# Kernel tuning notes

Measured on AMD Instinct MI355X. Metric: run time of the kernel, lower is better.

Reference implementation:

```python
import jax, jax.numpy as jnp
import numpy as np

B, S, D, H, MULT = 4, 2048, 768, 12, 4
HD = D // H
EPS = 1e-6


def _ln(x, g, b):
    mu = jnp.mean(x, axis=-1, keepdims=True)
    var = jnp.var(x, axis=-1, keepdims=True)
    return (x - mu) * jax.lax.rsqrt(var + EPS) * g + b


def setup_inputs() -> dict:
    key = jax.random.key(0)
    ks = jax.random.split(key, 12)
    sd = 0.02
    inp = {
        "x": jax.random.normal(ks[0], (B, S, D), dtype=jnp.float32),
        "mask": jnp.ones((B, 1, 1, S), dtype=jnp.int32),
        "Wq": jax.random.normal(ks[1], (D, D), dtype=jnp.float32) * sd,
        "bq": jnp.zeros((D,), dtype=jnp.float32),
        "Wk": jax.random.normal(ks[2], (D, D), dtype=jnp.float32) * sd,
        "bk": jnp.zeros((D,), dtype=jnp.float32),
        "Wv": jax.random.normal(ks[3], (D, D), dtype=jnp.float32) * sd,
        "bv": jnp.zeros((D,), dtype=jnp.float32),
        "Wo": jax.random.normal(ks[4], (D, D), dtype=jnp.float32) * sd,
        "bo": jnp.zeros((D,), dtype=jnp.float32),
        "W1": jax.random.normal(ks[5], (D, MULT * D), dtype=jnp.float32) * sd,
        "b1": jnp.zeros((MULT * D,), dtype=jnp.float32),
        "W2": jax.random.normal(ks[6], (MULT * D, D), dtype=jnp.float32) * sd,
        "b2": jnp.zeros((D,), dtype=jnp.float32),
        "g1": jnp.ones((D,), dtype=jnp.float32),
        "be1": jnp.zeros((D,), dtype=jnp.float32),
        "g2": jnp.ones((D,), dtype=jnp.float32),
        "be2": jnp.zeros((D,), dtype=jnp.float32),
    }
    return inp


def reference(x, mask, Wq, bq, Wk, bk, Wv, bv, Wo, bo, W1, b1, W2, b2, g1, be1, g2, be2):
    scale = HD ** -0.5
    # projections -> [B,H,S,HD]
    q = (x @ Wq + bq).reshape(B, S, H, HD).transpose(0, 2, 1, 3)
    k = (x @ Wk + bk).reshape(B, S, H, HD).transpose(0, 2, 1, 3)
    v = (x @ Wv + bv).reshape(B, S, H, HD).transpose(0, 2, 1, 3)
    scores = jnp.einsum("bhqd,bhkd->bhqk", q, k) * scale
    scores = jnp.where(mask == 0, -jnp.inf, scores)
    attn = jax.nn.softmax(scores, axis=-1)
    out = jnp.einsum("bhqk,bhkd->bhqd", attn, v)
    out = out.transpose(0, 2, 1, 3).reshape(B, S, D)
    mha = out @ Wo + bo
    # residual + LN
    h = _ln(mha + x, g1, be1)
    # FFN (dropout inactive in eval; GELU exact as torch nn.GELU default)
    ff = jax.nn.gelu(h @ W1 + b1, approximate=False) @ W2 + b2
    return _ln(ff + h, g2, be2)
```

## Files before the change

### kernel.cpp

```cpp
#include <hip/hip_runtime.h>
#include <hip/hip_bf16.h>
#include <math.h>

#define B_  4
#define S_  2048
#define D_  768
#define H_  12
#define HD_ 64
#define DF_ 3072
#define BS_ (B_*S_)

#define QSCALE 0.18033688011112042f

typedef __attribute__((ext_vector_type(8))) short short8;
typedef __attribute__((ext_vector_type(4))) float f32x4;

__device__ __forceinline__ unsigned short f2b(float f){
    unsigned int x = __float_as_uint(f);
    return (unsigned short)((x + 0x7fffu + ((x >> 16) & 1u)) >> 16);
}
__device__ __forceinline__ float b2f(unsigned short u){
    return __uint_as_float(((unsigned int)u) << 16);
}

typedef __attribute__((address_space(1))) void gvoid_t;
typedef __attribute__((address_space(3))) void lvoid_t;
__device__ __forceinline__ void gload_lds16(const unsigned short* g, unsigned short* l){
    __builtin_amdgcn_global_load_lds((gvoid_t*)g, (lvoid_t*)l, 16, 0, 0);
}

__global__ __launch_bounds__(256) void prep_kernel(
    const float* __restrict__ x,
    const float* __restrict__ Wq, const float* __restrict__ Wk,
    const float* __restrict__ Wv, const float* __restrict__ Wo,
    const float* __restrict__ W1, const float* __restrict__ W2,
    const float* __restrict__ bq, const float* __restrict__ bk, const float* __restrict__ bv,
    unsigned short* __restrict__ xb, unsigned short* __restrict__ wqkvT,
    unsigned short* __restrict__ woT, unsigned short* __restrict__ w1T,
    unsigned short* __restrict__ w2T, float* __restrict__ bqkv)
{
    const int NCVT = (BS_*D_)/256;
    int bid = blockIdx.x;
    if (bid < NCVT){
        int i = bid*256 + threadIdx.x;
        xb[i] = f2b(x[i]);
        return;
    }
    bid -= NCVT;
    __shared__ float t[32][33];
    const float* src; unsigned short* dst; int K, N, bx, by;
    if (bid < 4*576){
        int wsel = bid / 576, tt = bid % 576;
        bx = tt % 24; by = tt / 24; K = D_; N = D_;
        src = (wsel==0)?Wq:(wsel==1)?Wk:(wsel==2)?Wv:Wo;
        dst = (wsel<3) ? (wqkvT + (size_t)wsel*D_*D_) : woT;
    } else if (bid < 4*576 + 2304){
        int tt = bid - 4*576; bx = tt % 96; by = tt / 96; K = D_; N = DF_; src = W1; dst = w1T;
    } else if (bid < 4*576 + 2*2304){
        int tt = bid - 4*576 - 2304; bx = tt % 24; by = tt / 24; K = DF_; N = D_; src = W2; dst = w2T;
    } else {
        int i = (bid - (4*576 + 2*2304))*256 + threadIdx.x;
        if (i < 3*D_) bqkv[i] = (i < D_) ? bq[i] : (i < 2*D_) ? bk[i-D_] : bv[i-2*D_];
        return;
    }
    int tx = threadIdx.x & 31, ty = threadIdx.x >> 5;
    #pragma unroll
    for (int i = 0; i < 4; ++i)
        t[ty + i*8][tx] = src[(size_t)(by*32 + ty + i*8) * N + bx*32 + tx];
    __syncthreads();
    #pragma unroll
    for (int i = 0; i < 4; ++i)
        dst[(size_t)(bx*32 + ty + i*8) * K + by*32 + tx] = f2b(t[tx][ty + i*8]);
}

__global__ __launch_bounds__(256, 4) void gemm_tn(
    const unsigned short* __restrict__ A,
    const unsigned short* __restrict__ Bt,
    const float* __restrict__ bias,
    float* __restrict__ Cf,
    unsigned short* __restrict__ Cb,
    unsigned short* __restrict__ vtg,
    int M, int N, int K, int klen, int act)
{
    __shared__ __align__(16) unsigned short As[128*64];
    __shared__ __align__(16) unsigned short Bs[128*64];

    const int tid  = threadIdx.x;
    const int bz   = blockIdx.z;
    const int w    = tid >> 6, lane = tid & 63;
    const int l16  = lane & 15, quad = lane >> 4;
    const int wm   = (w >> 1) * 64, wn = (w & 1) * 64;
    const int kbeg = bz * klen;

    const int nwg = gridDim.x * gridDim.y;
    int wg = blockIdx.y * gridDim.x + blockIdx.x;
    wg = (wg & 7) * (nwg >> 3) + (wg >> 3);
    const int bn = wg % gridDim.x, bm = wg / gridDim.x;

    const unsigned short* Abase = A  + (size_t)bm * 128 * K;
    const unsigned short* Bbase = Bt + (size_t)bn * 128 * K;

    f32x4 acc[4][4] = {};

    for (int kt = kbeg; kt < kbeg + klen; kt += 64){
        #pragma unroll
        for (int c0 = 0; c0 < 4; ++c0){
            int c = tid + c0 * 256;
            int row = c >> 3, q = c & 7;
            int sw = (q ^ row) & 7;
            gload_lds16(Abase + (size_t)row * K + kt + sw*8, As + c*8);
            gload_lds16(Bbase + (size_t)row * K + kt + sw*8, Bs + c*8);
        }
        __syncthreads();

        #pragma unroll
        for (int kc = 0; kc < 2; ++kc){
            short8 af[4], bf[4];
            #pragma unroll
            for (int mi = 0; mi < 4; ++mi)
                af[mi] = *(const short8*)&As[(wm + mi*16 + l16)*64 + (((kc*4 + quad) ^ l16) & 7)*8];
            #pragma unroll
            for (int ni = 0; ni < 4; ++ni)
                bf[ni] = *(const short8*)&Bs[(wn + ni*16 + l16)*64 + (((kc*4 + quad) ^ l16) & 7)*8];
            #pragma unroll
            for (int mi = 0; mi < 4; ++mi)
                #pragma unroll
                for (int ni = 0; ni < 4; ++ni)
                    acc[mi][ni] = __builtin_amdgcn_mfma_f32_16x16x32_bf16(af[mi], bf[ni], acc[mi][ni], 0, 0, 0);
        }
        __syncthreads();
    }

    if (act == 2 && bn >= 12){
        #pragma unroll
        for (int mi = 0; mi < 4; ++mi){
            int rowbase = bm*128 + wm + mi*16 + quad*4;
            int bidx = rowbase >> 11, s0 = rowbase & 2047;
            int sp = (s0 & ~31) | (((s0 >> 2) & 3) << 3) | (((s0 >> 4) & 1) << 2);
            #pragma unroll
            for (int ni = 0; ni < 4; ++ni){
                int col  = bn*128 + wn + ni*16 + l16;
                int hcol = col - 2*D_;
                int hh   = hcol >> 6, dd = hcol & 63;
                float bia = bias ? bias[col] : 0.f;
                unsigned long long pk = 0;
                #pragma unroll
                for (int r = 0; r < 4; ++r)
                    pk |= (unsigned long long)f2b(acc[mi][ni][r] + bia) << (16*r);
                *(unsigned long long*)(vtg + (((size_t)bidx*H_ + hh)*64 + dd)*2048 + sp) = pk;
            }
        }
        return;
    }

    float* Cfz = Cf ? (Cf + (size_t)bz * M * N) : nullptr;
    const bool addb = (bias != nullptr) && (bz == 0);
    #pragma unroll
    for (int mi = 0; mi < 4; ++mi){
        #pragma unroll
        for (int ni = 0; ni < 4; ++ni){
            int col = bn*128 + wn + ni*16 + l16;
            float bia = addb ? bias[col] : 0.f;
            #pragma unroll
            for (int r = 0; r < 4; ++r){
                int row = bm*128 + wm + mi*16 + quad*4 + r;
                float v = acc[mi][ni][r] + bia;
                if (act == 1){
                    float u = v * (0.7978845608028654f + 0.0356774081f * v * v);
                    float e = __builtin_amdgcn_exp2f(u * 2.885390081777927f);
                    v = 0.5f * v * (1.f + (1.f - 2.f / (e + 1.f)));
                } else if (act == 2 && col < D_) v *= QSCALE;
                size_t idx = (size_t)row * N + col;
                if (Cfz) Cfz[idx] = v;
                if (Cb) Cb[idx] = f2b(v);
            }
        }
    }
}

__global__ __launch_bounds__(256, 3) void attn_kernel(
    const unsigned short* __restrict__ qkv,
    const unsigned short* __restrict__ vtg,
    const int* __restrict__ mask,
    unsigned short* __restrict__ ctx)
{
    __shared__ __align__(16) unsigned short Kl[128*64];
    __shared__ __align__(16) unsigned short Vt[64*128];

    const int tid = threadIdx.x;
    const int bid = blockIdx.x;
    const int hid = bid % 48;
    const int qb  = bid / 48;
    const int h   = hid % H_;
    const int b   = hid / H_;
    const int w   = tid >> 6, lane = tid & 63;
    const int l16 = lane & 15, quad = lane >> 4;
    const int q0  = qb * 128 + w * 32;
    const size_t base = (size_t)b * S_;
    const int hoff = h * HD_;

    short8 qf[2][2];
    #pragma unroll
    for (int g = 0; g < 2; ++g)
        #pragma unroll
        for (int kc = 0; kc < 2; ++kc)
            qf[g][kc] = *(const short8*)(qkv + (base + q0 + g*16 + l16)*2304 + hoff + kc*32 + quad*8);

    f32x4 o[2][4] = {};
    float l_s[2] = {0.f, 0.f};

    const unsigned short* vrow = vtg + ((size_t)(b*H_ + h) * 64) * 2048;

    for (int kt = 0; kt < S_/128; ++kt){
        __syncthreads();
        #pragma unroll
        for (int c0 = 0; c0 < 4; ++c0){
            int c = tid + c0*256;
            int rr = c >> 3, ch = c & 7;
            int sw = (ch ^ rr) & 7;
            gload_lds16(qkv + (base + kt*128 + rr)*2304 + D_ + hoff + sw*8, Kl + c*8);
            int d = c >> 4, pch = c & 15;
            int lch = (pch ^ d) & 15;
            gload_lds16(vrow + (size_t)d*2048 + kt*128 + lch*8, Vt + c*8);
        }
        __syncthreads();

        int mv0 = mask[b*S_ + kt*128 + lane];
        int mv1 = mask[b*S_ + kt*128 + 64 + lane];
        const bool allok = __all((mv0 != 0) && (mv1 != 0));

        #pragma unroll
        for (int t = 0; t < 4; ++t){
            short8 kf[2][2];
            #pragma unroll
            for (int kc = 0; kc < 2; ++kc){
                int co = (((kc*4 + quad) ^ l16) & 7)*8;
                kf[kc][0] = *(const short8*)&Kl[((2*t  )*16 + l16)*64 + co];
                kf[kc][1] = *(const short8*)&Kl[((2*t+1)*16 + l16)*64 + co];
            }
            short8 pks[2];
            #pragma unroll
            for (int g = 0; g < 2; ++g){
                f32x4 sf2[2] = {};
                #pragma unroll
                for (int kc = 0; kc < 2; ++kc){
                    sf2[0] = __builtin_amdgcn_mfma_f32_16x16x32_bf16(kf[kc][0], qf[g][kc], sf2[0], 0, 0, 0);
                    sf2[1] = __builtin_amdgcn_mfma_f32_16x16x32_bf16(kf[kc][1], qf[g][kc], sf2[1], 0, 0, 0);
                }
                if (!allok){
                    #pragma unroll
                    for (int j = 0; j < 2; ++j)
                        #pragma unroll
                        for (int r = 0; r < 4; ++r)
                            if (mask[b*S_ + kt*128 + (2*t+j)*16 + quad*4 + r] == 0)
                                sf2[j][r] = -1e30f;
                }
                #pragma unroll
                for (int j = 0; j < 2; ++j)
                    #pragma unroll
                    for (int r = 0; r < 4; ++r){
                        float p = __builtin_amdgcn_exp2f(sf2[j][r]);
                        sf2[j][r] = p; l_s[g] += p;
                    }
                union { unsigned int u[4]; short8 s; } pk;
                pk.u[0] = __builtin_amdgcn_perm(__float_as_uint(sf2[0][1]), __float_as_uint(sf2[0][0]), 0x07060302u);
                pk.u[1] = __builtin_amdgcn_perm(__float_as_uint(sf2[0][3]), __float_as_uint(sf2[0][2]), 0x07060302u);
                pk.u[2] = __builtin_amdgcn_perm(__float_as_uint(sf2[1][1]), __float_as_uint(sf2[1][0]), 0x07060302u);
                pk.u[3] = __builtin_amdgcn_perm(__float_as_uint(sf2[1][3]), __float_as_uint(sf2[1][2]), 0x07060302u);
                pks[g] = pk.s;
            }
            #pragma unroll
            for (int nt = 0; nt < 4; ++nt){
                int d = nt*16 + l16;
                short8 vf = *(const short8*)&Vt[d*128 + (((t*4 + quad) ^ l16) & 15)*8];
                o[0][nt] = __builtin_amdgcn_mfma_f32_16x16x32_bf16(pks[0], vf, o[0][nt], 0, 0, 0);
                o[1][nt] = __builtin_amdgcn_mfma_f32_16x16x32_bf16(pks[1], vf, o[1][nt], 0, 0, 0);
            }
        }
    }

    #pragma unroll
    for (int g = 0; g < 2; ++g){
        float ls = l_s[g];
        ls += __shfl_xor(ls, 16);
        ls += __shfl_xor(ls, 32);
        float linv[4];
        #pragma unroll
        for (int r = 0; r < 4; ++r)
            linv[r] = 1.f / __shfl(ls, quad*4 + r);
        #pragma unroll
        for (int nt = 0; nt < 4; ++nt)
            #pragma unroll
            for (int r = 0; r < 4; ++r){
                int qrow = q0 + g*16 + quad*4 + r;
                ctx[(base + qrow)*D_ + hoff + nt*16 + l16] = f2b(o[g][nt][r] * linv[r]);
            }
    }
}

__global__ __launch_bounds__(256) void ln_kernel(
    const float* __restrict__ inp, const float* __restrict__ inp2,
    const float* __restrict__ resf, const unsigned short* __restrict__ resb,
    const float* __restrict__ g, const float* __restrict__ be,
    float* __restrict__ outf, unsigned short* __restrict__ outb)
{
    const int row = blockIdx.x;
    const int tid = threadIdx.x;
    const float* ip = inp + (size_t)row * D_;
    const float* ip2 = inp2 ? inp2 + (size_t)row * D_ : nullptr;

    float v[3], s = 0.f, ss = 0.f;
    #pragma unroll
    for (int i = 0; i < 3; ++i){
        int c = tid + i*256;
        float x = ip[c];
        if (ip2) x += ip2[c];
        x += resf ? resf[(size_t)row * D_ + c] : b2f(resb[(size_t)row * D_ + c]);
        v[i] = x; s += x; ss += x * x;
    }
    #pragma unroll
    for (int d = 1; d < 64; d <<= 1){ s += __shfl_xor(s, d); ss += __shfl_xor(ss, d); }
    __shared__ float rs[4], rss[4];
    int w = tid >> 6;
    if ((tid & 63) == 0){ rs[w] = s; rss[w] = ss; }
    __syncthreads();
    s  = rs[0] + rs[1] + rs[2] + rs[3];
    ss = rss[0] + rss[1] + rss[2] + rss[3];
    float mu   = s * (1.f / 768.f);
    float var  = ss * (1.f / 768.f) - mu * mu;
    float rstd = rsqrtf(var + 1e-6f);
    #pragma unroll
    for (int i = 0; i < 3; ++i){
        int c = tid + i*256;
        float y = (v[i] - mu) * rstd * g[c] + be[c];
        if (outf) outf[(size_t)row * D_ + c] = y;
        if (outb) outb[(size_t)row * D_ + c] = f2b(y);
    }
}

extern "C" void kernel_launch(void* const* d_in, const int* in_sizes, int n_in,
                              void* d_out, int out_size, void* d_ws, size_t ws_size,
                              hipStream_t stream)
{
    const float* x    = (const float*)d_in[0];
    const int*   mask = (const int*)  d_in[1];
    const float* Wq   = (const float*)d_in[2];
    const float* bq   = (const float*)d_in[3];
    const float* Wk   = (const float*)d_in[4];
    const float* bk   = (const float*)d_in[5];
    const float* Wv   = (const float*)d_in[6];
    const float* bv   = (const float*)d_in[7];
    const float* Wo   = (const float*)d_in[8];
    const float* bo   = (const float*)d_in[9];
    const float* W1   = (const float*)d_in[10];
    const float* b1   = (const float*)d_in[11];
    const float* W2   = (const float*)d_in[12];
    const float* b2   = (const float*)d_in[13];
    const float* g1   = (const float*)d_in[14];
    const float* be1  = (const float*)d_in[15];
    const float* g2   = (const float*)d_in[16];
    const float* be2  = (const float*)d_in[17];
    float* out = (float*)d_out;
    (void)in_sizes; (void)n_in; (void)out_size; (void)ws_size;

    char* ws = (char*)d_ws;
    const size_t n_x = (size_t)BS_ * D_;

    size_t off = 0;
    auto take = [&](size_t bytes){ size_t o = off; off += (bytes + 255) & ~(size_t)255; return o; };
    unsigned short* xb    = (unsigned short*)(ws + take(n_x * 2));
    unsigned short* hb    = xb;
    unsigned short* wqkvT = (unsigned short*)(ws + take((size_t)3*D_*D_ * 2));
    unsigned short* woT   = (unsigned short*)(ws + take((size_t)D_*D_ * 2));
    unsigned short* w1T   = (unsigned short*)(ws + take((size_t)D_*DF_ * 2));
    unsigned short* w2T   = (unsigned short*)(ws + take((size_t)D_*DF_ * 2));
    float*          bqkv  = (float*)(ws + take((size_t)3*D_ * 4));
    size_t big = take((size_t)BS_ * 2304 * 2 + n_x * 2);
    unsigned short* qkvb = (unsigned short*)(ws + big);
    unsigned short* ctxb = qkvb + (size_t)BS_ * 2304;
    unsigned short* ff1b = qkvb;
    float* pf32 = (float*)(ws + take(2 * n_x * 4));
    float* mhaf = pf32;
    float* ff2f = pf32;
    unsigned short* vtg = (unsigned short*)(ws + take(n_x * 2));

    prep_kernel<<<24576 + 3*2304 + 9, 256, 0, stream>>>(
        x, Wq, Wk, Wv, Wo, W1, W2, bq, bk, bv,
        xb, wqkvT, woT, w1T, w2T, bqkv);

    dim3 blk(256);
    gemm_tn<<<dim3(18, 64, 1), blk, 0, stream>>>(xb, wqkvT, bqkv, nullptr, qkvb, vtg, BS_, 3*D_, D_, D_, 2);
    attn_kernel<<<B_ * H_ * (S_/128), 256, 0, stream>>>(qkvb, vtg, mask, ctxb);
    gemm_tn<<<dim3(6, 64, 2), blk, 0, stream>>>(ctxb, woT, bo, mhaf, nullptr, nullptr, BS_, D_, D_, D_/2, 0);
    ln_kernel<<<BS_, blk, 0, stream>>>(mhaf, mhaf + n_x, x, nullptr, g1, be1, nullptr, hb);
    gemm_tn<<<dim3(24, 64, 1), blk, 0, stream>>>(hb, w1T, b1, nullptr, ff1b, nullptr, BS_, DF_, D_, D_, 1);
    gemm_tn<<<dim3(6, 64, 2), blk, 0, stream>>>(ff1b, w2T, b2, ff2f, nullptr, nullptr, BS_, D_, DF_, DF_/2, 0);
    ln_kernel<<<BS_, blk, 0, stream>>>(ff2f, ff2f + n_x, nullptr, hb, g2, be2, out, nullptr);
}
```

Baseline: 389.6 us.

## Double-buffer attention K/V tiles and precompute mask bits with inline LDS reads

```diff
diff --git a/kernel.cpp b/kernel.cpp
--- a/kernel.cpp
+++ b/kernel.cpp
@@ -25,9 +25,15 @@
 
 typedef __attribute__((address_space(1))) void gvoid_t;
 typedef __attribute__((address_space(3))) void lvoid_t;
+typedef __attribute__((address_space(3))) unsigned char lchar_t;
 __device__ __forceinline__ void gload_lds16(const unsigned short* g, unsigned short* l){
     __builtin_amdgcn_global_load_lds((gvoid_t*)g, (lvoid_t*)l, 16, 0, 0);
 }
+__device__ __forceinline__ unsigned ldsaddr(const void* p){
+    return (unsigned)(size_t)(lchar_t*)(lvoid_t*)p;
+}
+#define DSR(dst, addr, OFF) \
+    asm volatile("ds_read_b128 %0, %1 offset:" #OFF : "=v"(dst) : "v"(addr))
 
 __global__ __launch_bounds__(256) void prep_kernel(
     const float* __restrict__ x,
@@ -184,8 +190,8 @@
     const int* __restrict__ mask,
     unsigned short* __restrict__ ctx)
 {
-    __shared__ __align__(16) unsigned short Kl[128*64];
-    __shared__ __align__(16) unsigned short Vt[64*128];
+    __shared__ __align__(16) unsigned short Kl[2*4096];
+    __shared__ __align__(16) unsigned short Vt[2*4096];
 
     const int tid = threadIdx.x;
     const int bid = blockIdx.x;
@@ -206,53 +212,71 @@
         for (int kc = 0; kc < 2; ++kc)
             qf[g][kc] = *(const short8*)(qkv + (base + q0 + g*16 + l16)*2304 + hoff + kc*32 + quad*8);
 
+    unsigned okbits = 0;
+    for (int kt = 0; kt < 32; ++kt){
+        int mv = mask[b*S_ + kt*64 + lane];
+        okbits |= (__all(mv != 0) ? (1u << kt) : 0u);
+    }
+
+    const unsigned short* vrow = vtg + ((size_t)(b*H_ + h) * 64) * 2048;
+
+    const int rrA  = tid >> 3, slA = tid & 7, swA = (slA ^ rrA) & 7;
+    const int koffA = rrA*2304 + hoff + swA*8;
+    const int voffA = rrA*2048 + swA*8;
+    unsigned short* kd = Kl + tid*8;
+    unsigned short* vd = Vt + tid*8;
+
+#define STAGE(_kt, _buf) do{ \
+    const unsigned short* kq = qkv + (base + (size_t)(_kt)*64)*2304 + D_; \
+    const unsigned short* vq = vrow + (_kt)*64; \
+    gload_lds16(kq + koffA,           kd + (_buf)*4096); \
+    gload_lds16(kq + koffA + 32*2304, kd + (_buf)*4096 + 2048); \
+    gload_lds16(vq + voffA,           vd + (_buf)*4096); \
+    gload_lds16(vq + voffA + 32*2048, vd + (_buf)*4096 + 2048); \
+}while(0)
+
+    const unsigned fb = (unsigned)(l16*128 + ((quad ^ l16) & 7)*16);
+    const unsigned kr0 = ldsaddr(Kl) + fb, kr1 = kr0 ^ 64u;
+    const unsigned vr0 = ldsaddr(Vt) + fb, vr1 = vr0 ^ 64u;
+
     f32x4 o[2][4] = {};
     float l_s[2] = {0.f, 0.f};
 
-    const unsigned short* vrow = vtg + ((size_t)(b*H_ + h) * 64) * 2048;
-
-    for (int kt = 0; kt < S_/128; ++kt){
-        __syncthreads();
-        #pragma unroll
-        for (int c0 = 0; c0 < 4; ++c0){
-            int c = tid + c0*256;
-            int rr = c >> 3, ch = c & 7;
-            int sw = (ch ^ rr) & 7;
-            gload_lds16(qkv + (base + kt*128 + rr)*2304 + D_ + hoff + sw*8, Kl + c*8);
-            int d = c >> 4, pch = c & 15;
-            int lch = (pch ^ d) & 15;
-            gload_lds16(vrow + (size_t)d*2048 + kt*128 + lch*8, Vt + c*8);
-        }
-        __syncthreads();
-
-        int mv0 = mask[b*S_ + kt*128 + lane];
-        int mv1 = mask[b*S_ + kt*128 + 64 + lane];
-        const bool allok = __all((mv0 != 0) && (mv1 != 0));
-
-        #pragma unroll
-        for (int t = 0; t < 4; ++t){
-            short8 kf[2][2];
-            #pragma unroll
-            for (int kc = 0; kc < 2; ++kc){
-                int co = (((kc*4 + quad) ^ l16) & 7)*8;
-                kf[kc][0] = *(const short8*)&Kl[((2*t  )*16 + l16)*64 + co];
-                kf[kc][1] = *(const short8*)&Kl[((2*t+1)*16 + l16)*64 + co];
-            }
+    STAGE(0, 0);
+    asm volatile("s_waitcnt vmcnt(0)" ::: "memory");
+    __builtin_amdgcn_sched_barrier(0);
+    __builtin_amdgcn_s_barrier();
+
+    for (int kt = 0; kt < 32; ++kt){
+        if (kt + 1 < 32) STAGE(kt + 1, (kt & 1) ^ 1);
+        const unsigned rb = (unsigned)(kt & 1) << 13;
+        const bool allok = (okbits >> kt) & 1u;
+
+        #pragma unroll
+        for (int t = 0; t < 2; ++t){
+            const unsigned ka0 = kr0 + rb + t*4096, ka1 = kr1 + rb + t*4096;
+            const unsigned va  = (t ? vr1 : vr0) + rb;
+            short8 kf00, kf01, kf10, kf11, vf[4];
+            DSR(kf00, ka0, 0); DSR(kf01, ka0, 2048);
+            DSR(kf10, ka1, 0); DSR(kf11, ka1, 2048);
+            DSR(vf[0], va, 0); DSR(vf[1], va, 2048); DSR(vf[2], va, 4096); DSR(vf[3], va, 6144);
+            asm volatile("s_waitcnt lgkmcnt(4)" ::: "memory");
+            __builtin_amdgcn_sched_barrier(0);
+
             short8 pks[2];
             #pragma unroll
             for (int g = 0; g < 2; ++g){
                 f32x4 sf2[2] = {};
-                #pragma unroll
-                for (int kc = 0; kc < 2; ++kc){
-                    sf2[0] = __builtin_amdgcn_mfma_f32_16x16x32_bf16(kf[kc][0], qf[g][kc], sf2[0], 0, 0, 0);
-                    sf2[1] = __builtin_amdgcn_mfma_f32_16x16x32_bf16(kf[kc][1], qf[g][kc], sf2[1], 0, 0, 0);
-                }
+                sf2[0] = __builtin_amdgcn_mfma_f32_16x16x32_bf16(kf00, qf[g][0], sf2[0], 0, 0, 0);
+                sf2[1] = __builtin_amdgcn_mfma_f32_16x16x32_bf16(kf01, qf[g][0], sf2[1], 0, 0, 0);
+                sf2[0] = __builtin_amdgcn_mfma_f32_16x16x32_bf16(kf10, qf[g][1], sf2[0], 0, 0, 0);
+                sf2[1] = __builtin_amdgcn_mfma_f32_16x16x32_bf16(kf11, qf[g][1], sf2[1], 0, 0, 0);
                 if (!allok){
                     #pragma unroll
                     for (int j = 0; j < 2; ++j)
                         #pragma unroll
                         for (int r = 0; r < 4; ++r)
-                            if (mask[b*S_ + kt*128 + (2*t+j)*16 + quad*4 + r] == 0)
+                            if (mask[b*S_ + kt*64 + (2*t+j)*16 + quad*4 + r] == 0)
                                 sf2[j][r] = -1e30f;
                 }
                 #pragma unroll
@@ -269,15 +293,20 @@
                 pk.u[3] = __builtin_amdgcn_perm(__float_as_uint(sf2[1][3]), __float_as_uint(sf2[1][2]), 0x07060302u);
                 pks[g] = pk.s;
             }
+            asm volatile("s_waitcnt lgkmcnt(0)" ::: "memory");
+            __builtin_amdgcn_sched_barrier(0);
             #pragma unroll
             for (int nt = 0; nt < 4; ++nt){
-                int d = nt*16 + l16;
-                short8 vf = *(const short8*)&Vt[d*128 + (((t*4 + quad) ^ l16) & 15)*8];
-                o[0][nt] = __builtin_amdgcn_mfma_f32_16x16x32_bf16(pks[0], vf, o[0][nt], 0, 0, 0);
-                o[1][nt] = __builtin_amdgcn_mfma_f32_16x16x32_bf16(pks[1], vf, o[1][nt], 0, 0, 0);
+                o[0][nt] = __builtin_amdgcn_mfma_f32_16x16x32_bf16(pks[0], vf[nt], o[0][nt], 0, 0, 0);
+                o[1][nt] = __builtin_amdgcn_mfma_f32_16x16x32_bf16(pks[1], vf[nt], o[1][nt], 0, 0, 0);
             }
         }
-    }
+
+        asm volatile("s_waitcnt vmcnt(0)" ::: "memory");
+        __builtin_amdgcn_sched_barrier(0);
+        __builtin_amdgcn_s_barrier();
+    }
+#undef STAGE
 
     #pragma unroll
     for (int g = 0; g < 2; ++g){
```

New measurement: 389.5 us. No clear change (-0.0%).
